# Optimization experiments

Measured on AMD Instinct MI355X. Metric: run time of the kernel, lower is better.

## Reference

```python
import jax, jax.numpy as jnp
import numpy as np

N = 100000   # nodes
E = 800000   # edges
F_IN = 256   # num_features
H = 256      # hidden_dim
C = 2        # num_classes
G = 128      # graphs in batch


def setup_inputs() -> dict:
    key = jax.random.key(0)
    ks = jax.random.split(key, 6)
    x = jax.random.normal(ks[0], (N, F_IN), jnp.float32)
    edge_index = jax.random.randint(ks[1], (2, E), 0, N, dtype=jnp.int64)
    # sorted graph ids, every one of the G graphs non-empty (global_max_pool needs no empty segments)
    batch = (jnp.arange(N, dtype=jnp.int64) * G) // N
    init = lambda k, shp, fan: jax.random.normal(k, shp, jnp.float32) / np.float32(np.sqrt(fan))
    W1 = init(ks[2], (F_IN, H), F_IN); b1 = jnp.zeros((H,), jnp.float32)
    W2 = init(ks[3], (H, H), H);       b2 = jnp.zeros((H,), jnp.float32)
    Wc = init(ks[4], (H, C), H);       bc = jnp.zeros((C,), jnp.float32)
    return dict(x=x, edge_index=edge_index, batch=batch,
                W1=W1, b1=b1, W2=W2, b2=b2, Wc=Wc, bc=bc)


def gcn_conv(x, W, b, row, col, n):
    """PyG GCNConv: h = D^-1/2 (A+I) D^-1/2 x W + b (row/col already include self-loops)."""
    h = x @ W                                                        # [n, out]
    deg = jax.ops.segment_sum(jnp.ones(col.shape, jnp.float32), col, num_segments=n)
    dinv = jnp.where(deg > 0, jax.lax.rsqrt(jnp.maximum(deg, 1.0)), 0.0)
    norm = dinv[row] * dinv[col]                                     # [E+n]
    out = jax.ops.segment_sum(h[row] * norm[:, None], col, num_segments=n)
    return out + b


def reference(x, edge_index, batch, W1, b1, W2, b2, Wc, bc):
    n = x.shape[0]
    loop = jnp.arange(n, dtype=edge_index.dtype)
    row = jnp.concatenate([edge_index[0], loop])   # add self-loops
    col = jnp.concatenate([edge_index[1], loop])
    h = jax.nn.relu(gcn_conv(x, W1, b1, row, col, n))
    # F.dropout(p=0.5) is identity in eval mode
    h = gcn_conv(h, W2, b2, row, col, n)
    g = jax.ops.segment_max(h, batch, num_segments=G)  # global_max_pool -> [G, H]
    logits = g @ Wc + bc
    return jax.nn.log_softmax(logits, axis=1)
```

## Files before the change

### kernel.cpp

```cpp
#include <hip/hip_runtime.h>
#include <hip/hip_bf16.h>

#define N_NODES 100000
#define N_EDGES 800000
#define HD 256
#define NG 128

__device__ __forceinline__ unsigned f2key(float f){
  unsigned u = __float_as_uint(f);
  return (u & 0x80000000u) ? ~u : (u | 0x80000000u);
}
__device__ __forceinline__ float key2f(unsigned k){
  unsigned u = (k & 0x80000000u) ? (k & 0x7FFFFFFFu) : ~k;
  return __uint_as_float(u);
}

__device__ __forceinline__ unsigned short f2bf(float f){
  unsigned u = __float_as_uint(f);
  unsigned r = (u + 0x7FFFu + ((u >> 16) & 1u)) >> 16;
  return (unsigned short)r;
}
__device__ __forceinline__ float bflo(unsigned u){ return __uint_as_float(u << 16); }
__device__ __forceinline__ float bfhi(unsigned u){ return __uint_as_float(u & 0xFFFF0000u); }

__global__ void k_deg(const int* __restrict__ ei, int* __restrict__ deg){
  int e = blockIdx.x*256 + threadIdx.x;
  const int M = N_EDGES + N_NODES;
  if(e < M){
    int c = (e < N_EDGES) ? ei[N_EDGES + e] : (e - N_EDGES);
    atomicAdd(&deg[c], 1);
  }
}

__global__ void k_scan1(const int* __restrict__ deg, int* __restrict__ ptr,
                        int* __restrict__ partials){
  __shared__ int s[256];
  int tid = threadIdx.x;
  int i = blockIdx.x*256 + tid;
  int v = (i < N_NODES) ? deg[i] : 0;
  s[tid] = v; __syncthreads();
  for(int off=1; off<256; off<<=1){
    int t = (tid >= off) ? s[tid-off] : 0;
    __syncthreads();
    s[tid] += t;
    __syncthreads();
  }
  if(i < N_NODES) ptr[i] = s[tid] - v;
  if(tid == 255) partials[blockIdx.x] = s[255];
}

__global__ void k_scan2(int* __restrict__ partials, int nb, int* __restrict__ ptrN){
  if(threadIdx.x == 0 && blockIdx.x == 0){
    int run = 0;
    for(int b=0;b<nb;b++){ int t = partials[b]; partials[b] = run; run += t; }
    *ptrN = run;
  }
}

__global__ void k_scan3(int* __restrict__ ptr, const int* __restrict__ partials,
                        int* __restrict__ cursor){
  int i = blockIdx.x*256 + threadIdx.x;
  if(i < N_NODES){
    int v = ptr[i] + partials[blockIdx.x];
    ptr[i] = v; cursor[i] = v;
  }
}

__global__ void k_fill(const int* __restrict__ ei, int* __restrict__ cursor,
                       int* __restrict__ src){
  int e = blockIdx.x*256 + threadIdx.x;
  const int M = N_EDGES + N_NODES;
  if(e < M){
    int r, c;
    if(e < N_EDGES){ r = ei[e]; c = ei[N_EDGES + e]; }
    else           { r = c = e - N_EDGES; }
    int pos = atomicAdd(&cursor[c], 1);
    src[pos] = r;
  }
}

__global__ void k_dinv(const int* __restrict__ deg, float* __restrict__ dinv){
  int i = blockIdx.x*256 + threadIdx.x;
  if(i < N_NODES) dinv[i] = rsqrtf((float)deg[i]);
}

__global__ __launch_bounds__(256) void k_gemm(const float* __restrict__ A,
                                              const float* __restrict__ W,
                                              const float* __restrict__ scale,
                                              unsigned short* __restrict__ out){
  __shared__ float As[16][132];
  __shared__ float Bs[16][132];
  int tid = threadIdx.x;
  int ty = tid >> 4, tx = tid & 15;
  float acc[8][8];
  #pragma unroll
  for(int i=0;i<8;i++)
    #pragma unroll
    for(int j=0;j<8;j++) acc[i][j] = 0.f;

  int ar = tid >> 1;
  int ac = (tid & 1) << 3;
  int grow = blockIdx.x*128 + ar;
  int brow = tid >> 4;
  int bcol = (tid & 15) << 3;
  const float* aptr = A + (size_t)grow*HD + ac;
  const float* bptr = W + (size_t)brow*HD + blockIdx.y*128 + bcol;
  bool aval = grow < N_NODES;

  for(int k0=0;k0<HD;k0+=16){
    float4 a0 = make_float4(0,0,0,0), a1 = a0;
    if(aval){ a0 = *(const float4*)(aptr); a1 = *(const float4*)(aptr+4); }
    float4 b0 = *(const float4*)(bptr);
    float4 b1 = *(const float4*)(bptr+4);
    aptr += 16; bptr += (size_t)16*HD;
    __syncthreads();
    As[ac+0][ar]=a0.x; As[ac+1][ar]=a0.y; As[ac+2][ar]=a0.z; As[ac+3][ar]=a0.w;
    As[ac+4][ar]=a1.x; As[ac+5][ar]=a1.y; As[ac+6][ar]=a1.z; As[ac+7][ar]=a1.w;
    *(float4*)&Bs[brow][bcol]   = b0;
    *(float4*)&Bs[brow][bcol+4] = b1;
    __syncthreads();
    #pragma unroll
    for(int kk=0;kk<16;kk++){
      float a[8], b[8];
      *(float4*)&a[0] = *(const float4*)&As[kk][ty*8];
      *(float4*)&a[4] = *(const float4*)&As[kk][ty*8+4];
      *(float4*)&b[0] = *(const float4*)&Bs[kk][tx*8];
      *(float4*)&b[4] = *(const float4*)&Bs[kk][tx*8+4];
      #pragma unroll
      for(int i=0;i<8;i++)
        #pragma unroll
        for(int j=0;j<8;j++) acc[i][j] = fmaf(a[i], b[j], acc[i][j]);
    }
  }
  int rowBase = blockIdx.x*128 + ty*8;
  int colBase = blockIdx.y*128 + tx*8;
  #pragma unroll
  for(int i=0;i<8;i++){
    int r = rowBase + i;
    if(r < N_NODES){
      float s = scale[r];
      ushort4 s0 = make_ushort4(f2bf(acc[i][0]*s), f2bf(acc[i][1]*s),
                                f2bf(acc[i][2]*s), f2bf(acc[i][3]*s));
      ushort4 s1 = make_ushort4(f2bf(acc[i][4]*s), f2bf(acc[i][5]*s),
                                f2bf(acc[i][6]*s), f2bf(acc[i][7]*s));
      *(ushort4*)(out + (size_t)r*HD + colBase)     = s0;
      *(ushort4*)(out + (size_t)r*HD + colBase + 4) = s1;
    }
  }
}

template<int RELU, int POOL>
__global__ __launch_bounds__(256) void k_agg(const unsigned short* __restrict__ t,
    const int* __restrict__ ptr, const int* __restrict__ src,
    const float* __restrict__ dinv, const float* __restrict__ bias,
    float* __restrict__ out, unsigned* __restrict__ gkeys,
    const int* __restrict__ batch){
  int v = blockIdx.x*4 + (threadIdx.x >> 6);
  if(v >= N_NODES) return;
  const int lane = threadIdx.x & 63;
  const unsigned short* tl = t + lane*4;

  int j0 = ptr[v], j1 = ptr[v+1];
  float dv = dinv[v];
  int f = lane*4;
  float4 b4 = *(const float4*)(bias + f);
  int gidx = 0;
  if(POOL) gidx = batch[v];

  float ax=0.f, ay=0.f, az=0.f, aw=0.f;
  const int last = j1 - 1;

  for(int j=j0; j<j1; j+=8){
    int jc1=j+1>last?last:j+1, jc2=j+2>last?last:j+2, jc3=j+3>last?last:j+3;
    int jc4=j+4>last?last:j+4, jc5=j+5>last?last:j+5, jc6=j+6>last?last:j+6;
    int jc7=j+7>last?last:j+7;
    int i0=src[j],   i1=src[jc1], i2=src[jc2], i3=src[jc3];
    int i4=src[jc4], i5=src[jc5], i6=src[jc6], i7=src[jc7];
    float w1=(j+1<j1)?1.f:0.f, w2=(j+2<j1)?1.f:0.f, w3=(j+3<j1)?1.f:0.f;
    float w4=(j+4<j1)?1.f:0.f, w5=(j+5<j1)?1.f:0.f, w6=(j+6<j1)?1.f:0.f;
    float w7=(j+7<j1)?1.f:0.f;

    const unsigned short* p0 = tl + (size_t)i0*HD;
    const unsigned short* p1 = tl + (size_t)i1*HD;
    const unsigned short* p2 = tl + (size_t)i2*HD;
    const unsigned short* p3 = tl + (size_t)i3*HD;
    const unsigned short* p4 = tl + (size_t)i4*HD;
    const unsigned short* p5 = tl + (size_t)i5*HD;
    const unsigned short* p6 = tl + (size_t)i6*HD;
    const unsigned short* p7 = tl + (size_t)i7*HD;

    uint2 d0,d1,d2,d3,d4,d5,d6,d7;
    asm volatile("global_load_dwordx2 %0, %1, off" : "=v"(d0) : "v"(p0));
    asm volatile("global_load_dwordx2 %0, %1, off" : "=v"(d1) : "v"(p1));
    asm volatile("global_load_dwordx2 %0, %1, off" : "=v"(d2) : "v"(p2));
    asm volatile("global_load_dwordx2 %0, %1, off" : "=v"(d3) : "v"(p3));
    asm volatile("global_load_dwordx2 %0, %1, off" : "=v"(d4) : "v"(p4));
    asm volatile("global_load_dwordx2 %0, %1, off" : "=v"(d5) : "v"(p5));
    asm volatile("global_load_dwordx2 %0, %1, off" : "=v"(d6) : "v"(p6));
    asm volatile("global_load_dwordx2 %0, %1, off" : "=v"(d7) : "v"(p7));
    asm volatile("s_waitcnt vmcnt(0)" ::: "memory");
    __builtin_amdgcn_sched_barrier(0);

    ax += bflo(d0.x); ay += bfhi(d0.x); az += bflo(d0.y); aw += bfhi(d0.y);
    ax = fmaf(w1, bflo(d1.x), ax); ay = fmaf(w1, bfhi(d1.x), ay);
    az = fmaf(w1, bflo(d1.y), az); aw = fmaf(w1, bfhi(d1.y), aw);
    ax = fmaf(w2, bflo(d2.x), ax); ay = fmaf(w2, bfhi(d2.x), ay);
    az = fmaf(w2, bflo(d2.y), az); aw = fmaf(w2, bfhi(d2.y), aw);
    ax = fmaf(w3, bflo(d3.x), ax); ay = fmaf(w3, bfhi(d3.x), ay);
    az = fmaf(w3, bflo(d3.y), az); aw = fmaf(w3, bfhi(d3.y), aw);
    ax = fmaf(w4, bflo(d4.x), ax); ay = fmaf(w4, bfhi(d4.x), ay);
    az = fmaf(w4, bflo(d4.y), az); aw = fmaf(w4, bfhi(d4.y), aw);
    ax = fmaf(w5, bflo(d5.x), ax); ay = fmaf(w5, bfhi(d5.x), ay);
    az = fmaf(w5, bflo(d5.y), az); aw = fmaf(w5, bfhi(d5.y), aw);
    ax = fmaf(w6, bflo(d6.x), ax); ay = fmaf(w6, bfhi(d6.x), ay);
    az = fmaf(w6, bflo(d6.y), az); aw = fmaf(w6, bfhi(d6.y), aw);
    ax = fmaf(w7, bflo(d7.x), ax); ay = fmaf(w7, bfhi(d7.x), ay);
    az = fmaf(w7, bflo(d7.y), az); aw = fmaf(w7, bfhi(d7.y), aw);
  }

  float4 acc;
  acc.x = fmaf(ax, dv, b4.x);
  acc.y = fmaf(ay, dv, b4.y);
  acc.z = fmaf(az, dv, b4.z);
  acc.w = fmaf(aw, dv, b4.w);
  if(RELU){
    acc.x = fmaxf(acc.x, 0.f); acc.y = fmaxf(acc.y, 0.f);
    acc.z = fmaxf(acc.z, 0.f); acc.w = fmaxf(acc.w, 0.f);
  }
  if(POOL){
    unsigned* gp = gkeys + (size_t)gidx*HD + f;
    atomicMax(gp+0, f2key(acc.x));
    atomicMax(gp+1, f2key(acc.y));
    atomicMax(gp+2, f2key(acc.z));
    atomicMax(gp+3, f2key(acc.w));
  } else {
    *(float4*)(out + (size_t)v*HD + f) = acc;
  }
}

__global__ void k_head(const unsigned* __restrict__ gk, const float* __restrict__ Wc,
                       const float* __restrict__ bc, float* __restrict__ out){
  int i = threadIdx.x;
  if(i >= NG) return;
  float a0 = 0.f, a1 = 0.f;
  for(int k=0;k<HD;k++){
    float gv = key2f(gk[(size_t)i*HD + k]);
    a0 = fmaf(gv, Wc[2*k],   a0);
    a1 = fmaf(gv, Wc[2*k+1], a1);
  }
  a0 += bc[0]; a1 += bc[1];
  float m = fmaxf(a0, a1);
  float lse = m + logf(expf(a0-m) + expf(a1-m));
  out[2*i]   = a0 - lse;
  out[2*i+1] = a1 - lse;
}

extern "C" void kernel_launch(void* const* d_in, const int* in_sizes, int n_in,
                              void* d_out, int out_size, void* d_ws, size_t ws_size,
                              hipStream_t stream){
  (void)in_sizes; (void)n_in; (void)out_size; (void)ws_size;
  const float* x   = (const float*)d_in[0];
  const int*   ei  = (const int*)d_in[1];
  const int*   bat = (const int*)d_in[2];
  const float* W1  = (const float*)d_in[3];
  const float* b1  = (const float*)d_in[4];
  const float* W2  = (const float*)d_in[5];
  const float* b2  = (const float*)d_in[6];
  const float* Wc  = (const float*)d_in[7];
  const float* bc  = (const float*)d_in[8];
  float* out = (float*)d_out;

  char* ws = (char*)d_ws;
  size_t off = 0;
  auto alloc = [&](size_t bytes)->void*{
    void* p = ws + off; off = (off + bytes + 255) & ~(size_t)255; return p;
  };
  unsigned short* T = (unsigned short*)alloc((size_t)N_NODES*HD*2);
  float*    Hb     = (float*)alloc((size_t)N_NODES*HD*4);
  int*      deg    = (int*)alloc((size_t)N_NODES*4);
  float*    dinv   = (float*)alloc((size_t)N_NODES*4);
  int*      ptr    = (int*)alloc((size_t)(N_NODES+1)*4);
  int*      cursor = (int*)alloc((size_t)N_NODES*4);
  int*      src    = (int*)alloc((size_t)(N_EDGES+N_NODES)*4);
  int*      partials = (int*)alloc(512*4);
  unsigned* gkeys  = (unsigned*)alloc((size_t)NG*HD*4);

  const int M = N_EDGES + N_NODES;
  const int nbM = (M + 255)/256;
  const int nbN = (N_NODES + 255)/256;

  hipMemsetAsync(deg,   0, (size_t)N_NODES*4, stream);
  hipMemsetAsync(gkeys, 0, (size_t)NG*HD*4,   stream);

  k_deg  <<<nbM, 256, 0, stream>>>(ei, deg);
  k_scan1<<<nbN, 256, 0, stream>>>(deg, ptr, partials);
  k_scan2<<<1,   64,  0, stream>>>(partials, nbN, ptr + N_NODES);
  k_scan3<<<nbN, 256, 0, stream>>>(ptr, partials, cursor);
  k_fill <<<nbM, 256, 0, stream>>>(ei, cursor, src);
  k_dinv <<<nbN, 256, 0, stream>>>(deg, dinv);

  dim3 ggrid((N_NODES + 127)/128, HD/128);
  k_gemm<<<ggrid, 256, 0, stream>>>(x, W1, dinv, T);
  k_agg<1,0><<<(N_NODES+3)/4, 256, 0, stream>>>(T, ptr, src, dinv, b1, Hb, nullptr, nullptr);
  k_gemm<<<ggrid, 256, 0, stream>>>(Hb, W2, dinv, T);
  k_agg<0,1><<<(N_NODES+3)/4, 256, 0, stream>>>(T, ptr, src, dinv, b2, nullptr, gkeys, bat);
  k_head<<<1, 128, 0, stream>>>(gkeys, Wc, bc, out);
}
```

Baseline: 1.222 ms.

## Split wavefront into two half-waves gathering alternate edges with 16-byte loads

Each 64-lane wave now splits into two 32-lane halves. Each lane loads 8 bf16 features with dwordx4, and the two halves handle interleaved edges, then combine their partial sums with a cross-half shuffle. A special path for degree up to 8 issues only four loads per lane, which cuts the padded redundant loads for the common low-degree nodes. The goal is wider memory transactions and more edge-level parallelism, at the cost of more registers and a shuffle reduction.

```diff
diff --git a/kernel.cpp b/kernel.cpp
--- a/kernel.cpp
+++ b/kernel.cpp
@@ -149,6 +149,12 @@
   }
 }
 
+#define ACC8(D_,WT_) \
+  a0 = fmaf(WT_, bflo((D_).x), a0); a1 = fmaf(WT_, bfhi((D_).x), a1); \
+  a2 = fmaf(WT_, bflo((D_).y), a2); a3 = fmaf(WT_, bfhi((D_).y), a3); \
+  a4 = fmaf(WT_, bflo((D_).z), a4); a5 = fmaf(WT_, bfhi((D_).z), a5); \
+  a6 = fmaf(WT_, bflo((D_).w), a6); a7 = fmaf(WT_, bfhi((D_).w), a7);
+
 template<int RELU, int POOL>
 __global__ __launch_bounds__(256) void k_agg(const unsigned short* __restrict__ t,
     const int* __restrict__ ptr, const int* __restrict__ src,
@@ -158,83 +164,107 @@
   int v = blockIdx.x*4 + (threadIdx.x >> 6);
   if(v >= N_NODES) return;
   const int lane = threadIdx.x & 63;
-  const unsigned short* tl = t + lane*4;
+  const int half = lane >> 5;
+  const int sub  = lane & 31;
+  const unsigned short* tl = t + sub*8;
 
   int j0 = ptr[v], j1 = ptr[v+1];
   float dv = dinv[v];
-  int f = lane*4;
-  float4 b4 = *(const float4*)(bias + f);
   int gidx = 0;
   if(POOL) gidx = batch[v];
-
-  float ax=0.f, ay=0.f, az=0.f, aw=0.f;
   const int last = j1 - 1;
-
-  for(int j=j0; j<j1; j+=8){
-    int jc1=j+1>last?last:j+1, jc2=j+2>last?last:j+2, jc3=j+3>last?last:j+3;
-    int jc4=j+4>last?last:j+4, jc5=j+5>last?last:j+5, jc6=j+6>last?last:j+6;
-    int jc7=j+7>last?last:j+7;
-    int i0=src[j],   i1=src[jc1], i2=src[jc2], i3=src[jc3];
-    int i4=src[jc4], i5=src[jc5], i6=src[jc6], i7=src[jc7];
-    float w1=(j+1<j1)?1.f:0.f, w2=(j+2<j1)?1.f:0.f, w3=(j+3<j1)?1.f:0.f;
-    float w4=(j+4<j1)?1.f:0.f, w5=(j+5<j1)?1.f:0.f, w6=(j+6<j1)?1.f:0.f;
-    float w7=(j+7<j1)?1.f:0.f;
-
+  int deg = j1 - j0;
+
+  float a0=0.f,a1=0.f,a2=0.f,a3=0.f,a4=0.f,a5=0.f,a6=0.f,a7=0.f;
+
+  if(deg <= 8){
+    int e0 = j0 + half, e1 = e0 + 2, e2 = e0 + 4, e3 = e0 + 6;
+    float w0 = e0 < j1 ? 1.f : 0.f, w1 = e1 < j1 ? 1.f : 0.f;
+    float w2 = e2 < j1 ? 1.f : 0.f, w3 = e3 < j1 ? 1.f : 0.f;
+    int i0 = src[e0 > last ? last : e0];
+    int i1 = src[e1 > last ? last : e1];
+    int i2 = src[e2 > last ? last : e2];
+    int i3 = src[e3 > last ? last : e3];
     const unsigned short* p0 = tl + (size_t)i0*HD;
     const unsigned short* p1 = tl + (size_t)i1*HD;
     const unsigned short* p2 = tl + (size_t)i2*HD;
     const unsigned short* p3 = tl + (size_t)i3*HD;
-    const unsigned short* p4 = tl + (size_t)i4*HD;
-    const unsigned short* p5 = tl + (size_t)i5*HD;
-    const unsigned short* p6 = tl + (size_t)i6*HD;
-    const unsigned short* p7 = tl + (size_t)i7*HD;
-
-    uint2 d0,d1,d2,d3,d4,d5,d6,d7;
-    asm volatile("global_load_dwordx2 %0, %1, off" : "=v"(d0) : "v"(p0));
-    asm volatile("global_load_dwordx2 %0, %1, off" : "=v"(d1) : "v"(p1));
-    asm volatile("global_load_dwordx2 %0, %1, off" : "=v"(d2) : "v"(p2));
-    asm volatile("global_load_dwordx2 %0, %1, off" : "=v"(d3) : "v"(p3));
-    asm volatile("global_load_dwordx2 %0, %1, off" : "=v"(d4) : "v"(p4));
-    asm volatile("global_load_dwordx2 %0, %1, off" : "=v"(d5) : "v"(p5));
-    asm volatile("global_load_dwordx2 %0, %1, off" : "=v"(d6) : "v"(p6));
-    asm volatile("global_load_dwordx2 %0, %1, off" : "=v"(d7) : "v"(p7));
+    uint4 d0,d1,d2,d3;
+    asm volatile("global_load_dwordx4 %0, %1, off" : "=v"(d0) : "v"(p0));
+    asm volatile("global_load_dwordx4 %0, %1, off" : "=v"(d1) : "v"(p1));
+    asm volatile("global_load_dwordx4 %0, %1, off" : "=v"(d2) : "v"(p2));
+    asm volatile("global_load_dwordx4 %0, %1, off" : "=v"(d3) : "v"(p3));
     asm volatile("s_waitcnt vmcnt(0)" ::: "memory");
     __builtin_amdgcn_sched_barrier(0);
-
-    ax += bflo(d0.x); ay += bfhi(d0.x); az += bflo(d0.y); aw += bfhi(d0.y);
-    ax = fmaf(w1, bflo(d1.x), ax); ay = fmaf(w1, bfhi(d1.x), ay);
-    az = fmaf(w1, bflo(d1.y), az); aw = fmaf(w1, bfhi(d1.y), aw);
-    ax = fmaf(w2, bflo(d2.x), ax); ay = fmaf(w2, bfhi(d2.x), ay);
-    az = fmaf(w2, bflo(d2.y), az); aw = fmaf(w2, bfhi(d2.y), aw);
-    ax = fmaf(w3, bflo(d3.x), ax); ay = fmaf(w3, bfhi(d3.x), ay);
-    az = fmaf(w3, bflo(d3.y), az); aw = fmaf(w3, bfhi(d3.y), aw);
-    ax = fmaf(w4, bflo(d4.x), ax); ay = fmaf(w4, bfhi(d4.x), ay);
-    az = fmaf(w4, bflo(d4.y), az); aw = fmaf(w4, bfhi(d4.y), aw);
-    ax = fmaf(w5, bflo(d5.x), ax); ay = fmaf(w5, bfhi(d5.x), ay);
-    az = fmaf(w5, bflo(d5.y), az); aw = fmaf(w5, bfhi(d5.y), aw);
-    ax = fmaf(w6, bflo(d6.x), ax); ay = fmaf(w6, bfhi(d6.x), ay);
-    az = fmaf(w6, bflo(d6.y), az); aw = fmaf(w6, bfhi(d6.y), aw);
-    ax = fmaf(w7, bflo(d7.x), ax); ay = fmaf(w7, bfhi(d7.x), ay);
-    az = fmaf(w7, bflo(d7.y), az); aw = fmaf(w7, bfhi(d7.y), aw);
-  }
-
-  float4 acc;
-  acc.x = fmaf(ax, dv, b4.x);
-  acc.y = fmaf(ay, dv, b4.y);
-  acc.z = fmaf(az, dv, b4.z);
-  acc.w = fmaf(aw, dv, b4.w);
+    ACC8(d0,w0) ACC8(d1,w1) ACC8(d2,w2) ACC8(d3,w3)
+  } else {
+    for(int j=j0; j<j1; j+=16){
+      int e0 = j + half, e1 = e0 + 2, e2 = e0 + 4, e3 = e0 + 6;
+      int e4 = e0 + 8, e5 = e0 + 10, e6 = e0 + 12, e7 = e0 + 14;
+      float w0 = e0 < j1 ? 1.f : 0.f, w1 = e1 < j1 ? 1.f : 0.f;
+      float w2 = e2 < j1 ? 1.f : 0.f, w3 = e3 < j1 ? 1.f : 0.f;
+      float w4 = e4 < j1 ? 1.f : 0.f, w5 = e5 < j1 ? 1.f : 0.f;
+      float w6 = e6 < j1 ? 1.f : 0.f, w7 = e7 < j1 ? 1.f : 0.f;
+      int i0 = src[e0 > last ? last : e0];
+      int i1 = src[e1 > last ? last : e1];
+      int i2 = src[e2 > last ? last : e2];
+      int i3 = src[e3 > last ? last : e3];
+      int i4 = src[e4 > last ? last : e4];
+      int i5 = src[e5 > last ? last : e5];
+      int i6 = src[e6 > last ? last : e6];
+      int i7 = src[e7 > last ? last : e7];
+      const unsigned short* p0 = tl + (size_t)i0*HD;
+      const unsigned short* p1 = tl + (size_t)i1*HD;
+      const unsigned short* p2 = tl + (size_t)i2*HD;
+      const unsigned short* p3 = tl + (size_t)i3*HD;
+      const unsigned short* p4 = tl + (size_t)i4*HD;
+      const unsigned short* p5 = tl + (size_t)i5*HD;
+      const unsigned short* p6 = tl + (size_t)i6*HD;
+      const unsigned short* p7 = tl + (size_t)i7*HD;
+      uint4 d0,d1,d2,d3,d4,d5,d6,d7;
+      asm volatile("global_load_dwordx4 %0, %1, off" : "=v"(d0) : "v"(p0));
+      asm volatile("global_load_dwordx4 %0, %1, off" : "=v"(d1) : "v"(p1));
+      asm volatile("global_load_dwordx4 %0, %1, off" : "=v"(d2) : "v"(p2));
+      asm volatile("global_load_dwordx4 %0, %1, off" : "=v"(d3) : "v"(p3));
+      asm volatile("global_load_dwordx4 %0, %1, off" : "=v"(d4) : "v"(p4));
+      asm volatile("global_load_dwordx4 %0, %1, off" : "=v"(d5) : "v"(p5));
+      asm volatile("global_load_dwordx4 %0, %1, off" : "=v"(d6) : "v"(p6));
+      asm volatile("global_load_dwordx4 %0, %1, off" : "=v"(d7) : "v"(p7));
+      asm volatile("s_waitcnt vmcnt(0)" ::: "memory");
+      __builtin_amdgcn_sched_barrier(0);
+      ACC8(d0,w0) ACC8(d1,w1) ACC8(d2,w2) ACC8(d3,w3)
+      ACC8(d4,w4) ACC8(d5,w5) ACC8(d6,w6) ACC8(d7,w7)
+    }
+  }
+
+  a0 += __shfl_xor(a0, 32); a1 += __shfl_xor(a1, 32);
+  a2 += __shfl_xor(a2, 32); a3 += __shfl_xor(a3, 32);
+  a4 += __shfl_xor(a4, 32); a5 += __shfl_xor(a5, 32);
+  a6 += __shfl_xor(a6, 32); a7 += __shfl_xor(a7, 32);
+
+  int f = sub*8;
+  float4 blo = *(const float4*)(bias + f);
+  float4 bhi = *(const float4*)(bias + f + 4);
+  float r0 = fmaf(a0, dv, blo.x), r1 = fmaf(a1, dv, blo.y);
+  float r2 = fmaf(a2, dv, blo.z), r3 = fmaf(a3, dv, blo.w);
+  float r4 = fmaf(a4, dv, bhi.x), r5 = fmaf(a5, dv, bhi.y);
+  float r6 = fmaf(a6, dv, bhi.z), r7 = fmaf(a7, dv, bhi.w);
   if(RELU){
-    acc.x = fmaxf(acc.x, 0.f); acc.y = fmaxf(acc.y, 0.f);
-    acc.z = fmaxf(acc.z, 0.f); acc.w = fmaxf(acc.w, 0.f);
+    r0=fmaxf(r0,0.f); r1=fmaxf(r1,0.f); r2=fmaxf(r2,0.f); r3=fmaxf(r3,0.f);
+    r4=fmaxf(r4,0.f); r5=fmaxf(r5,0.f); r6=fmaxf(r6,0.f); r7=fmaxf(r7,0.f);
   }
   if(POOL){
-    unsigned* gp = gkeys + (size_t)gidx*HD + f;
-    atomicMax(gp+0, f2key(acc.x));
-    atomicMax(gp+1, f2key(acc.y));
-    atomicMax(gp+2, f2key(acc.z));
-    atomicMax(gp+3, f2key(acc.w));
+    unsigned* gp = gkeys + (size_t)gidx*HD + f + half*4;
+    if(half == 0){
+      atomicMax(gp+0, f2key(r0)); atomicMax(gp+1, f2key(r1));
+      atomicMax(gp+2, f2key(r2)); atomicMax(gp+3, f2key(r3));
+    } else {
+      atomicMax(gp+0, f2key(r4)); atomicMax(gp+1, f2key(r5));
+      atomicMax(gp+2, f2key(r6)); atomicMax(gp+3, f2key(r7));
+    }
   } else {
-    *(float4*)(out + (size_t)v*HD + f) = acc;
+    float4 wv = half ? make_float4(r4,r5,r6,r7) : make_float4(r0,r1,r2,r3);
+    *(float4*)(out + (size_t)v*HD + f + half*4) = wv;
   }
 }
 
```

Result: slower. 1.381 ms (+13.1%).
